# Kernel optimization log

Hardware: AMD Instinct MI355X
Metric: run time of the kernel (lower is better)

Reference implementation:

```python
import jax, jax.numpy as jnp
import numpy as np

HIDDEN = 1024
NUM_BLOCKS = 8
BLOCK = HIDDEN // NUM_BLOCKS  # 128
EPS = 1e-6


def cayley_batch(A):
    # A: [b, r, r] -> orthogonal Q = (I - S) @ inv(I + S + eps*I), S = 0.5*(A - A^T)
    b, r, _ = A.shape
    I = jnp.eye(r, dtype=A.dtype)
    S = 0.5 * (A - jnp.swapaxes(A, -2, -1))
    return jnp.matmul(I - S, jnp.linalg.inv(I + S + EPS * I))


def apply_block_diag(W, R):
    # W @ block_diag(R_0..R_{n-1}) without materializing the hidden x hidden matrix.
    # W: [out, hidden], R: [n, bs, bs]
    out = W.shape[0]
    Wb = W.reshape(out, NUM_BLOCKS, BLOCK)
    return jnp.einsum('onb,nbc->onc', Wb, R).reshape(out, NUM_BLOCKS * BLOCK)


def setup_inputs() -> dict:
    key = jax.random.key(0)
    ks = jax.random.split(key, 6)
    return {
        'attn_weight': jax.random.normal(ks[0], (3 * HIDDEN, HIDDEN), dtype=jnp.float32) * 0.02,
        'bias': jax.random.normal(ks[1], (3 * HIDDEN,), dtype=jnp.float32) * 0.02,
        'x': jax.random.normal(ks[2], (8, 4096, HIDDEN), dtype=jnp.float32),
        'q_R': jax.random.normal(ks[3], (NUM_BLOCKS, BLOCK, BLOCK), dtype=jnp.float32),
        'k_R': jax.random.normal(ks[4], (NUM_BLOCKS, BLOCK, BLOCK), dtype=jnp.float32),
        'v_R': jax.random.normal(ks[5], (NUM_BLOCKS, BLOCK, BLOCK), dtype=jnp.float32),
    }


def reference(attn_weight, bias, x, q_R, k_R, v_R):
    orth_q = cayley_batch(q_R)
    orth_k = cayley_batch(k_R)
    orth_v = cayley_batch(v_R)
    q_w, k_w, v_w = jnp.split(attn_weight, 3, axis=0)  # each [hidden, hidden]
    filt_q = apply_block_diag(q_w, orth_q)
    filt_k = apply_block_diag(k_w, orth_k)
    filt_v = apply_block_diag(v_w, orth_v)
    filt = jnp.concatenate([filt_q, filt_k, filt_v], axis=0)  # [3*hidden, hidden]
    # F.linear: x @ filt^T + bias -> [B, S, 3*hidden]
    return jnp.einsum('bsh,oh->bso', x, filt) + bias
```

## Files before the change

kernel.cpp:

```cpp
#include <hip/hip_runtime.h>

typedef __bf16 bf16x8 __attribute__((ext_vector_type(8)));
typedef float  f32x4  __attribute__((ext_vector_type(4)));

#define EPSC 1e-6f

__device__ __forceinline__ unsigned short f2bf(float f) {
  union { float f; unsigned int u; } c; c.f = f;
  unsigned int u = c.u;
  u = u + 0x7FFFu + ((u >> 16) & 1u);
  return (unsigned short)(u >> 16);
}
__device__ __forceinline__ float bf2f(unsigned short h) {
  union { unsigned int u; float f; } c; c.u = ((unsigned int)h) << 16;
  return c.f;
}
__device__ __forceinline__ void gl_lds16(const unsigned short* g, unsigned short* l) {
  __builtin_amdgcn_global_load_lds((const __attribute__((address_space(1))) void*)g,
                                   (__attribute__((address_space(3))) void*)l, 16, 0, 0);
}

__global__ void __launch_bounds__(512) cayley_cvt_k(const float* __restrict__ qR,
                                                    const float* __restrict__ kR,
                                                    const float* __restrict__ vR,
                                                    float* __restrict__ wsL,
                                                    float* __restrict__ wsQt,
                                                    const float4* __restrict__ xin,
                                                    ushort4* __restrict__ xbf,
                                                    int n4) {
  extern __shared__ float A_s[];
  const int tid = threadIdx.x;

  if (blockIdx.x >= 24) {
    int i = (blockIdx.x - 24) * 512 + tid;
    int stride = (gridDim.x - 24) * 512;
    for (; i < n4; i += stride) {
      float4 v = xin[i];
      ushort4 o;
      o.x = f2bf(v.x); o.y = f2bf(v.y); o.z = f2bf(v.z); o.w = f2bf(v.w);
      xbf[i] = o;
    }
    return;
  }

  float4* A4 = (float4*)A_s;
  const int m = blockIdx.x;
  const float* R = (m < 8 ? qR : (m < 16 ? kR : vR)) + (size_t)(m & 7) * 16384;
  float* Lg = wsL  + (size_t)m * 16384;
  float* Qt = wsQt + (size_t)m * 16384;

  for (int idx = tid; idx < 16384; idx += 512) {
    int i = idx >> 7, j = idx & 127;
    float s = 0.5f * (R[idx] - R[j * 128 + i]);
    float v = ((i == j) ? (1.0f + EPSC) : 0.0f) - s;
    A_s[idx] = v;
    Lg[idx] = v;
  }

  const int c = tid & 31;
  const int rg = tid >> 5;
  for (int k = 0; k < 128; ++k) {
    __syncthreads();
    if (tid < 32) {
      float ip = 1.0f / A_s[k * 128 + k];
      float4 v = A4[k * 32 + tid];
      v.x *= ip; v.y *= ip; v.z *= ip; v.w *= ip;
      if (tid == (k >> 2)) {
        int k3 = k & 3;
        if (k3 == 0) v.x = ip; else if (k3 == 1) v.y = ip;
        else if (k3 == 2) v.z = ip; else v.w = ip;
      }
      A4[k * 32 + tid] = v;
    }
    __syncthreads();

    float4 rk = A4[k * 32 + c];
    const int kc = k >> 2, k3 = k & 3;
    const float ipv = (k3 == 0) ? rk.x : (k3 == 1) ? rk.y : (k3 == 2) ? rk.z : rk.w;

    float mi[8];
    float4 v[8];
#pragma unroll
    for (int p = 0; p < 8; ++p) mi[p] = A_s[(p * 16 + rg) * 128 + k];
#pragma unroll
    for (int p = 0; p < 8; ++p) v[p] = A4[(p * 16 + rg) * 32 + c];
#pragma unroll
    for (int p = 0; p < 8; ++p) {
      const int i = p * 16 + rg;
      const bool isk = (i == k);
      const float mm = isk ? 0.0f : mi[p];
      float4 w = v[p];
      w.x -= mm * rk.x; w.y -= mm * rk.y; w.z -= mm * rk.z; w.w -= mm * rk.w;
      if (c == kc && !isk) {
        const float fx = -mm * ipv;
        if (k3 == 0) w.x = fx; else if (k3 == 1) w.y = fx;
        else if (k3 == 2) w.z = fx; else w.w = fx;
      }
      A4[i * 32 + c] = w;
    }
  }
  __syncthreads();

  const int ti = tid >> 4, tj = tid & 15;
  const int i0 = ti * 4, j0 = tj * 8;
  float acc[4][8];
#pragma unroll
  for (int r = 0; r < 4; ++r)
#pragma unroll
    for (int s = 0; s < 8; ++s) acc[r][s] = 0.f;

  for (int tc = 0; tc < 32; ++tc) {
    float4 b4[8];
#pragma unroll
    for (int s = 0; s < 8; ++s)
      b4[s] = *(const float4*)&Lg[(size_t)(j0 + s) * 128 + tc * 4];
#pragma unroll
    for (int r = 0; r < 4; ++r) {
      float4 a4 = A4[(i0 + r) * 32 + tc];
#pragma unroll
      for (int s = 0; s < 8; ++s)
        acc[r][s] += a4.x * b4[s].x + a4.y * b4[s].y + a4.z * b4[s].z + a4.w * b4[s].w;
    }
  }
#pragma unroll
  for (int r = 0; r < 4; ++r)
#pragma unroll
    for (int s = 0; s < 8; ++s) {
      float v = acc[r][s] - EPSC * A_s[(i0 + r) * 128 + j0 + s];
      Qt[(size_t)(i0 + r) * 128 + j0 + s] = v;
    }
}

__global__ void __launch_bounds__(256) filt_k(const float* __restrict__ W,
                                              const float* __restrict__ wsQt,
                                              unsigned short* __restrict__ filt) {
  __shared__ unsigned short Qs[128 * 136];
  const int m = blockIdx.x;
  const int ot = blockIdx.y;
  const int mset = m >> 3, n = m & 7;
  const float* Qt = wsQt + (size_t)m * 16384;
  const int tid = threadIdx.x;

  for (int idx = tid; idx < 16384; idx += 256) {
    int i = idx >> 7, j = idx & 127;
    Qs[i * 136 + j] = f2bf(Qt[idx]);
  }
  __syncthreads();

  const int ol = tid & 63, cg = tid >> 6;
  const int go = mset * 1024 + ot * 64 + ol;
  const float* Wrow = W + (size_t)go * 1024 + n * 128;

  float acc[32];
#pragma unroll
  for (int i = 0; i < 32; ++i) acc[i] = 0.f;

  for (int b4 = 0; b4 < 32; ++b4) {
    float4 w4 = *(const float4*)(Wrow + b4 * 4);
#pragma unroll
    for (int cc = 0; cc < 32; ++cc) {
      int cidx = cg * 32 + cc;
      ushort4 q4 = *(const ushort4*)&Qs[cidx * 136 + b4 * 4];
      acc[cc] += w4.x * bf2f(q4.x) + w4.y * bf2f(q4.y)
               + w4.z * bf2f(q4.z) + w4.w * bf2f(q4.w);
    }
  }
  unsigned short* dst = filt + (size_t)go * 1024 + n * 128 + cg * 32;
#pragma unroll
  for (int g2 = 0; g2 < 8; ++g2) {
    ushort4 o;
    o.x = f2bf(acc[g2 * 4 + 0]); o.y = f2bf(acc[g2 * 4 + 1]);
    o.z = f2bf(acc[g2 * 4 + 2]); o.w = f2bf(acc[g2 * 4 + 3]);
    *(ushort4*)(dst + g2 * 4) = o;
  }
}

__global__ void __launch_bounds__(256) gemm_k(const unsigned short* __restrict__ Ax,
                                              const unsigned short* __restrict__ Bf,
                                              const float* __restrict__ bias,
                                              float* __restrict__ C) {
  __shared__ unsigned short As[128 * 32];
  __shared__ unsigned short Bs[128 * 32];
  const int tid = threadIdx.x;
  const int bx = blockIdx.x;
  const int by = blockIdx.y;
  const int lane = tid & 63, wave = tid >> 6;
  const int wm = wave & 1, wn = wave >> 1;
  const int quad = lane >> 4, l16 = lane & 15;
  const long mbase = (long)by * 128;
  const long nbase = (long)bx * 128;

  f32x4 acc[4][4];
#pragma unroll
  for (int i = 0; i < 4; ++i)
#pragma unroll
    for (int j = 0; j < 4; ++j) {
      acc[i][j][0] = 0.f; acc[i][j][1] = 0.f; acc[i][j][2] = 0.f; acc[i][j][3] = 0.f;
    }

  const int q0 = tid, q1 = 256 + tid;
  const int row0 = q0 >> 2, c0 = (q0 & 3) * 8;
  const int row1 = q1 >> 2, c1 = (q1 & 3) * 8;
  const unsigned short* a0 = Ax + (mbase + row0) * 1024 + c0;
  const unsigned short* a1 = Ax + (mbase + row1) * 1024 + c1;
  const unsigned short* b0 = Bf + (nbase + row0) * 1024 + c0;
  const unsigned short* b1 = Bf + (nbase + row1) * 1024 + c1;
  unsigned short* lA0 = &As[q0 * 8]; unsigned short* lA1 = &As[q1 * 8];
  unsigned short* lB0 = &Bs[q0 * 8]; unsigned short* lB1 = &Bs[q1 * 8];

  for (int kk = 0; kk < 1024; kk += 32) {
    gl_lds16(a0 + kk, lA0);
    gl_lds16(a1 + kk, lA1);
    gl_lds16(b0 + kk, lB0);
    gl_lds16(b1 + kk, lB1);
    __syncthreads();

    bf16x8 af[4], bff[4];
#pragma unroll
    for (int mi = 0; mi < 4; ++mi)
      af[mi] = *(const bf16x8*)&As[(wm * 64 + mi * 16 + l16) * 32 + quad * 8];
#pragma unroll
    for (int ni = 0; ni < 4; ++ni)
      bff[ni] = *(const bf16x8*)&Bs[(wn * 64 + ni * 16 + l16) * 32 + quad * 8];
#pragma unroll
    for (int mi = 0; mi < 4; ++mi)
#pragma unroll
      for (int ni = 0; ni < 4; ++ni)
        acc[mi][ni] = __builtin_amdgcn_mfma_f32_16x16x32_bf16(af[mi], bff[ni], acc[mi][ni], 0, 0, 0);
    __syncthreads();
  }

#pragma unroll
  for (int ni = 0; ni < 4; ++ni) {
    long gcol = nbase + wn * 64 + ni * 16 + l16;
    float bv = bias[gcol];
#pragma unroll
    for (int mi = 0; mi < 4; ++mi) {
      long grow = mbase + wm * 64 + mi * 16 + quad * 4;
#pragma unroll
      for (int r = 0; r < 4; ++r)
        C[(grow + r) * 3072 + gcol] = acc[mi][ni][r] + bv;
    }
  }
}

extern "C" void kernel_launch(void* const* d_in, const int* in_sizes, int n_in,
                              void* d_out, int out_size, void* d_ws, size_t ws_size,
                              hipStream_t stream) {
  const float* W    = (const float*)d_in[0];
  const float* bias = (const float*)d_in[1];
  const float* x    = (const float*)d_in[2];
  const float* qR   = (const float*)d_in[3];
  const float* kR   = (const float*)d_in[4];
  const float* vR   = (const float*)d_in[5];
  float* out = (float*)d_out;

  char* ws = (char*)d_ws;
  float* wsL           = (float*)(ws);
  float* wsQt          = (float*)(ws + 1572864);
  unsigned short* wsF  = (unsigned short*)(ws + 3145728);
  unsigned short* wsX  = (unsigned short*)(ws + 9437184);

  cayley_cvt_k<<<24 + 2048, 512, 65536, stream>>>(qR, kR, vR, wsL, wsQt,
                                                  (const float4*)x, (ushort4*)wsX,
                                                  33554432 / 4);
  filt_k<<<dim3(24, 16), 256, 0, stream>>>(W, wsQt, wsF);
  gemm_k<<<dim3(24, 256), 256, 0, stream>>>(wsX, wsF, bias, out);
}
```

Measured before the change: 915.8 us.

## Rewrite GEMM with 256x256 tiles, 4-stage async LDS pipeline and swizzle

The bf16 GEMM moves from 128x128 tiles with 256 threads to 256x256 tiles with 512 threads, and keeps a 4-buffer ring of direct global-to-LDS loads in 128KB of dynamic shared memory. Explicit vmcnt waits let loads run two stages ahead of the MFMA work, replacing the old load, sync, compute, sync loop. An XOR swizzle on LDS offsets is meant to avoid bank conflicts, and s_setprio raises wave priority around the MFMA block. The larger tiles cut global traffic per FLOP, at the cost of more registers, lower occupancy, and a single __syncthreads-free barrier per step whose correctness depends on the ring depth.

After: 872.1 us. -4.8%, faster.

```diff
diff --git a/kernel.cpp b/kernel.cpp
--- a/kernel.cpp
+++ b/kernel.cpp
@@ -18,6 +18,12 @@
 __device__ __forceinline__ void gl_lds16(const unsigned short* g, unsigned short* l) {
   __builtin_amdgcn_global_load_lds((const __attribute__((address_space(1))) void*)g,
                                    (__attribute__((address_space(3))) void*)l, 16, 0, 0);
+}
+
+template<int N> __device__ __forceinline__ void waitvm() {
+  if constexpr (N == 8)      asm volatile("s_waitcnt vmcnt(8)" ::: "memory");
+  else if constexpr (N == 4) asm volatile("s_waitcnt vmcnt(4)" ::: "memory");
+  else                       asm volatile("s_waitcnt vmcnt(0)" ::: "memory");
 }
 
 __global__ void __launch_bounds__(512) cayley_cvt_k(const float* __restrict__ qR,
@@ -175,68 +181,108 @@
   }
 }
 
-__global__ void __launch_bounds__(256) gemm_k(const unsigned short* __restrict__ Ax,
-                                              const unsigned short* __restrict__ Bf,
-                                              const float* __restrict__ bias,
-                                              float* __restrict__ C) {
-  __shared__ unsigned short As[128 * 32];
-  __shared__ unsigned short Bs[128 * 32];
+__global__ void __launch_bounds__(512, 2) gemm_k(const unsigned short* __restrict__ Ax,
+                                                 const unsigned short* __restrict__ Bf,
+                                                 const float* __restrict__ bias,
+                                                 float* __restrict__ C) {
+  extern __shared__ char smem_g[];
   const int tid = threadIdx.x;
-  const int bx = blockIdx.x;
-  const int by = blockIdx.y;
   const int lane = tid & 63, wave = tid >> 6;
   const int wm = wave & 1, wn = wave >> 1;
   const int quad = lane >> 4, l16 = lane & 15;
-  const long mbase = (long)by * 128;
-  const long nbase = (long)bx * 128;
-
-  f32x4 acc[4][4];
-#pragma unroll
-  for (int i = 0; i < 4; ++i)
-#pragma unroll
-    for (int j = 0; j < 4; ++j) {
-      acc[i][j][0] = 0.f; acc[i][j][1] = 0.f; acc[i][j][2] = 0.f; acc[i][j][3] = 0.f;
-    }
-
-  const int q0 = tid, q1 = 256 + tid;
-  const int row0 = q0 >> 2, c0 = (q0 & 3) * 8;
-  const int row1 = q1 >> 2, c1 = (q1 & 3) * 8;
-  const unsigned short* a0 = Ax + (mbase + row0) * 1024 + c0;
-  const unsigned short* a1 = Ax + (mbase + row1) * 1024 + c1;
-  const unsigned short* b0 = Bf + (nbase + row0) * 1024 + c0;
-  const unsigned short* b1 = Bf + (nbase + row1) * 1024 + c1;
-  unsigned short* lA0 = &As[q0 * 8]; unsigned short* lA1 = &As[q1 * 8];
-  unsigned short* lB0 = &Bs[q0 * 8]; unsigned short* lB1 = &Bs[q1 * 8];
-
-  for (int kk = 0; kk < 1024; kk += 32) {
-    gl_lds16(a0 + kk, lA0);
-    gl_lds16(a1 + kk, lA1);
-    gl_lds16(b0 + kk, lB0);
-    gl_lds16(b1 + kk, lB1);
-    __syncthreads();
-
-    bf16x8 af[4], bff[4];
-#pragma unroll
-    for (int mi = 0; mi < 4; ++mi)
-      af[mi] = *(const bf16x8*)&As[(wm * 64 + mi * 16 + l16) * 32 + quad * 8];
-#pragma unroll
-    for (int ni = 0; ni < 4; ++ni)
-      bff[ni] = *(const bf16x8*)&Bs[(wn * 64 + ni * 16 + l16) * 32 + quad * 8];
-#pragma unroll
-    for (int mi = 0; mi < 4; ++mi)
-#pragma unroll
-      for (int ni = 0; ni < 4; ++ni)
-        acc[mi][ni] = __builtin_amdgcn_mfma_f32_16x16x32_bf16(af[mi], bff[ni], acc[mi][ni], 0, 0, 0);
-    __syncthreads();
-  }
+  const long mbase = (long)blockIdx.y * 256;
+  const long nbase = (long)blockIdx.x * 256;
+
+  const unsigned short* gA0; const unsigned short* gA1;
+  const unsigned short* gB0; const unsigned short* gB1;
+  int dof0, dof1;
+  {
+    int D0 = 0 * 8192 + tid * 16;
+    int D1 = 1 * 8192 + tid * 16;
+    int L0 = D0 ^ (((D0 >> 7) & 3) << 4);
+    int L1 = D1 ^ (((D1 >> 7) & 3) << 4);
+    int r0 = L0 >> 6, c0 = (L0 & 63) >> 1;
+    int r1 = L1 >> 6, c1 = (L1 & 63) >> 1;
+    gA0 = Ax + (size_t)(mbase + r0) * 1024 + c0;
+    gA1 = Ax + (size_t)(mbase + r1) * 1024 + c1;
+    gB0 = Bf + (size_t)(nbase + r0) * 1024 + c0;
+    gB1 = Bf + (size_t)(nbase + r1) * 1024 + c1;
+    dof0 = D0; dof1 = D1;
+  }
+
+  int aoff[8], boff[4];
+#pragma unroll
+  for (int mi = 0; mi < 8; ++mi) {
+    int row = wm * 128 + mi * 16 + l16;
+    int L = row * 64 + quad * 16;
+    aoff[mi] = L ^ (((L >> 7) & 3) << 4);
+  }
+#pragma unroll
+  for (int ni = 0; ni < 4; ++ni) {
+    int row = wn * 64 + ni * 16 + l16;
+    int L = row * 64 + quad * 16;
+    boff[ni] = 16384 + (L ^ (((L >> 7) & 3) << 4));
+  }
+
+  f32x4 acc[8][4];
+#pragma unroll
+  for (int mi = 0; mi < 8; ++mi)
+#pragma unroll
+    for (int ni = 0; ni < 4; ++ni) {
+      acc[mi][ni][0] = 0.f; acc[mi][ni][1] = 0.f;
+      acc[mi][ni][2] = 0.f; acc[mi][ni][3] = 0.f;
+    }
+
+#define GSTAGE(T)                                                              \
+  {                                                                            \
+    char* sb = smem_g + ((T) & 3) * 32768;                                     \
+    gl_lds16(gA0 + (T) * 32, (unsigned short*)(sb + dof0));                    \
+    gl_lds16(gA1 + (T) * 32, (unsigned short*)(sb + dof1));                    \
+    gl_lds16(gB0 + (T) * 32, (unsigned short*)(sb + 16384 + dof0));            \
+    gl_lds16(gB1 + (T) * 32, (unsigned short*)(sb + 16384 + dof1));            \
+  }
+
+#define GSTEP(T, VM)                                                           \
+  {                                                                            \
+    waitvm<VM>();                                                              \
+    __builtin_amdgcn_s_barrier();                                              \
+    asm volatile("" ::: "memory");                                             \
+    const char* bb = smem_g + ((T) & 3) * 32768;                               \
+    bf16x8 bfr[4], afr[8];                                                     \
+    _Pragma("unroll")                                                          \
+    for (int ni = 0; ni < 4; ++ni) bfr[ni] = *(const bf16x8*)(bb + boff[ni]);  \
+    _Pragma("unroll")                                                          \
+    for (int mi = 0; mi < 8; ++mi) afr[mi] = *(const bf16x8*)(bb + aoff[mi]);  \
+    __builtin_amdgcn_s_setprio(1);                                             \
+    _Pragma("unroll")                                                          \
+    for (int mi = 0; mi < 8; ++mi)                                             \
+      _Pragma("unroll")                                                        \
+      for (int ni = 0; ni < 4; ++ni)                                           \
+        acc[mi][ni] = __builtin_amdgcn_mfma_f32_16x16x32_bf16(                 \
+            afr[mi], bfr[ni], acc[mi][ni], 0, 0, 0);                           \
+    __builtin_amdgcn_s_setprio(0);                                             \
+  }
+
+  GSTAGE(0);
+  GSTAGE(1);
+
+  for (int t = 0; t < 30; ++t) {
+    GSTAGE(t + 2);
+    GSTEP(t, 8);
+  }
+  GSTEP(30, 4);
+  GSTEP(31, 0);
+
+#undef GSTAGE
+#undef GSTEP
 
 #pragma unroll
   for (int ni = 0; ni < 4; ++ni) {
     long gcol = nbase + wn * 64 + ni * 16 + l16;
     float bv = bias[gcol];
 #pragma unroll
-    for (int mi = 0; mi < 4; ++mi) {
-      long grow = mbase + wm * 64 + mi * 16 + quad * 4;
+    for (int mi = 0; mi < 8; ++mi) {
+      long grow = mbase + wm * 128 + mi * 16 + quad * 4;
 #pragma unroll
       for (int r = 0; r < 4; ++r)
         C[(grow + r) * 3072 + gcol] = acc[mi][ni][r] + bv;
@@ -261,9 +307,16 @@
   unsigned short* wsF  = (unsigned short*)(ws + 3145728);
   unsigned short* wsX  = (unsigned short*)(ws + 9437184);
 
+  static bool attr_done = false;
+  if (!attr_done) {
+    (void)hipFuncSetAttribute(reinterpret_cast<const void*>(gemm_k),
+                              hipFuncAttributeMaxDynamicSharedMemorySize, 131072);
+    attr_done = true;
+  }
+
   cayley_cvt_k<<<24 + 2048, 512, 65536, stream>>>(qR, kR, vR, wsL, wsQt,
                                                   (const float4*)x, (ushort4*)wsX,
                                                   33554432 / 4);
   filt_k<<<dim3(24, 16), 256, 0, stream>>>(W, wsQt, wsF);
-  gemm_k<<<dim3(24, 256), 256, 0, stream>>>(wsX, wsF, bias, out);
-}
+  gemm_k<<<dim3(12, 128), 512, 131072, stream>>>(wsX, wsF, bias, out);
+}
```
